# Kernel tuning notes

Hardware: AMD Instinct MI355X
Metric: run time of the kernel (lower is better)

Reference implementation:

```python
import jax, jax.numpy as jnp
import numpy as np
from jax import lax

B = 16
T_MEL = 16
FEAT = 80
BITS = 9
N_CLASSES = 2 ** BITS  # 512
RNN = 512
SCALES = (5, 5, 11)
PAD = 2
TOTAL_SCALE = 275      # prod(SCALES)
INDENT = PAD * TOTAL_SCALE  # 550
T = (T_MEL - 2 * PAD) * TOTAL_SCALE  # 3300
D_IN = FEAT + N_CLASSES  # 592 = GRU input size


def setup_inputs() -> dict:
    key = jax.random.key(0)
    ks = jax.random.split(key, 10)
    s = 0.05
    inp = {
        "x": jax.random.randint(ks[0], (B, T), 0, N_CLASSES),
        "mels": jax.random.normal(ks[1], (B, FEAT, T_MEL), jnp.float32),
    }
    # upsample conv kernels: Conv2d(1,1,(1,2s+1)) with weight filled 1/(2s+1)
    for i, sc in enumerate(SCALES):
        k = 2 * sc + 1
        inp[f"up_k{i}"] = jnp.full((1, 1, 1, k), 1.0 / k, jnp.float32)
    # GRU (torch layout: [3H, in], gates ordered r,z,n)
    inp["w_ih"] = jax.random.normal(ks[2], (3 * RNN, D_IN), jnp.float32) * s
    inp["w_hh"] = jax.random.normal(ks[3], (3 * RNN, RNN), jnp.float32) * s
    inp["b_ih"] = jax.random.normal(ks[4], (3 * RNN,), jnp.float32) * s
    inp["b_hh"] = jax.random.normal(ks[5], (3 * RNN,), jnp.float32) * s
    # fc1: Linear(rnn_dims, n_classes); fc2: Linear(n_classes, n_classes)
    inp["fc1_w"] = jax.random.normal(ks[6], (N_CLASSES, RNN), jnp.float32) * s
    inp["fc1_b"] = jax.random.normal(ks[7], (N_CLASSES,), jnp.float32) * s
    inp["fc2_w"] = jax.random.normal(ks[8], (N_CLASSES, N_CLASSES), jnp.float32) * s
    inp["fc2_b"] = jax.random.normal(ks[9], (N_CLASSES,), jnp.float32) * s
    return inp


def _upsample_mels(mels, kernels):
    # m-path of UpsampleNetwork: Stretch2d(scale,1) + averaging Conv2d per scale
    m = mels[:, None]  # [B,1,FEAT,T_MEL]
    for sc, k in zip(SCALES, kernels):
        m = jnp.repeat(m, sc, axis=-1)  # Stretch2d along time
        m = lax.conv_general_dilated(
            m, k, window_strides=(1, 1), padding=[(0, 0), (sc, sc)],
            dimension_numbers=("NCHW", "OIHW", "NCHW"))
    m = m[:, 0, :, INDENT:-INDENT]  # [B, FEAT, T]
    return jnp.transpose(m, (0, 2, 1))  # [B, T, FEAT]


def _gru(xin, w_ih, w_hh, b_ih, b_hh):
    # precompute input projection for all timesteps: [B,T,3H]
    x_proj = jnp.einsum("btd,gd->btg", xin, w_ih) + b_ih

    def step(h, xp):  # xp: [B,3H]
        hp = h @ w_hh.T + b_hh
        xr, xz, xn = jnp.split(xp, 3, axis=-1)
        hr, hz, hn = jnp.split(hp, 3, axis=-1)
        r = jax.nn.sigmoid(xr + hr)
        z = jax.nn.sigmoid(xz + hz)
        n = jnp.tanh(xn + r * hn)
        h_new = (1.0 - z) * n + z * h
        return h_new, h_new

    h0 = jnp.zeros((xin.shape[0], RNN), xin.dtype)
    _, hs = lax.scan(step, h0, jnp.transpose(x_proj, (1, 0, 2)))  # [T,B,H]
    return jnp.transpose(hs, (1, 0, 2))  # [B,T,H]


def reference(x, mels, up_k0, up_k1, up_k2,
              w_ih, w_hh, b_ih, b_hh, fc1_w, fc1_b, fc2_w, fc2_b):
    # vectorized replacement for the per-element scatter loop: one-hot of x
    netinput = jax.nn.one_hot(x, N_CLASSES, dtype=jnp.float32)  # [B,T,C]
    mels_up = _upsample_mels(mels, (up_k0, up_k1, up_k2))       # [B,T,FEAT]
    xin = jnp.concatenate([netinput, mels_up], axis=2)          # [B,T,C+FEAT]
    h = _gru(xin, w_ih, w_hh, b_ih, b_hh)                       # [B,T,RNN]
    h = jax.nn.relu(jnp.einsum("bth,fh->btf", h, fc1_w) + fc1_b)
    out = jnp.einsum("btf,cf->btc", h, fc2_w) + fc2_b           # [B,T,C]
    return out
```

## Files before the change

### kernel.cpp

```cpp
#include <hip/hip_runtime.h>
#include <stdint.h>

typedef unsigned short ushort_t;
typedef unsigned long long u64;
typedef __attribute__((ext_vector_type(8))) short short8;
typedef __attribute__((ext_vector_type(4))) float f32x4;

#define T_SEQ 3300
#define SENT 0x7FC00001u
#define SENTPAIR 0x7FC000017FC00001ull

__device__ __forceinline__ ushort_t f2b(float f) {
  uint32_t u = __float_as_uint(f);
  u = (u + 0x7fffu + ((u >> 16) & 1u)) >> 16;
  return (ushort_t)u;
}
__device__ __forceinline__ float b2f(ushort_t b) {
  return __uint_as_float(((uint32_t)b) << 16);
}

__global__ void prep_kernel(const float* __restrict__ w_ih,
                            const float* __restrict__ fc1w,
                            const float* __restrict__ fc2w,
                            ushort_t* __restrict__ w_ihT,
                            ushort_t* __restrict__ fc1wb,
                            ushort_t* __restrict__ fc2wb,
                            uint32_t* __restrict__ h_ring) {
  int i = blockIdx.x * 256 + threadIdx.x;
  if (i < 512 * 1536) {
    int d = i / 1536, g = i - d * 1536;
    w_ihT[i] = f2b(w_ih[g * 592 + d]);
  }
  int j = i - 512 * 1536;
  if (j >= 0 && j < 262144) fc1wb[j] = f2b(fc1w[j]);
  int k = j - 262144;
  if (k >= 0 && k < 262144) fc2wb[k] = f2b(fc2w[k]);
  int c = k - 262144;
  if (c >= 0 && c < 131072) {
    __hip_atomic_store(&h_ring[c], SENT, __ATOMIC_RELAXED, __HIP_MEMORY_SCOPE_AGENT);
  }
}

__global__ void upsample_kernel(const float* __restrict__ mels,
                                const float* __restrict__ k0,
                                const float* __restrict__ k1,
                                const float* __restrict__ k2,
                                float* __restrict__ mels_up) {
  __shared__ float s0[16];
  __shared__ float s1[80];
  __shared__ float s2[400];
  int bf = blockIdx.x;
  int b = bf / 80, f = bf - b * 80;
  int tid = threadIdx.x;
  float c0 = k0[0], c1 = k1[0], c2 = k2[0];
  if (tid < 16) s0[tid] = mels[(b * 80 + f) * 16 + tid];
  __syncthreads();
  if (tid < 80) {
    float a = 0.f;
    #pragma unroll
    for (int d = -5; d <= 5; ++d) {
      int w = tid + d;
      if (w >= 0 && w < 80) a += s0[w / 5];
    }
    s1[tid] = a * c0;
  }
  __syncthreads();
  for (int w = tid; w < 400; w += 128) {
    float a = 0.f;
    #pragma unroll
    for (int d = -5; d <= 5; ++d) {
      int u = w + d;
      if (u >= 0 && u < 400) a += s1[u / 5];
    }
    s2[w] = a * c1;
  }
  __syncthreads();
  for (int t = tid; t < T_SEQ; t += 128) {
    int wb = 550 + t;
    float a = 0.f;
    #pragma unroll
    for (int d = -11; d <= 11; ++d) a += s2[(wb + d) / 11];
    mels_up[(b * 80 + f) * T_SEQ + t] = a * c2;
  }
}

__device__ __forceinline__ float red32(float x) {
  x += __uint_as_float((uint32_t)__builtin_amdgcn_update_dpp(0, (int)__float_as_uint(x), 0x111, 0xf, 0xf, true));
  x += __uint_as_float((uint32_t)__builtin_amdgcn_update_dpp(0, (int)__float_as_uint(x), 0x112, 0xf, 0xf, true));
  x += __uint_as_float((uint32_t)__builtin_amdgcn_update_dpp(0, (int)__float_as_uint(x), 0x114, 0xf, 0xf, true));
  x += __uint_as_float((uint32_t)__builtin_amdgcn_update_dpp(0, (int)__float_as_uint(x), 0x118, 0xf, 0xf, true));
  x += __shfl_xor(x, 16, 64);
  return x;
}

__global__ __launch_bounds__(512) void gru_kernel(
    const int* __restrict__ x,
    const float* __restrict__ mels_up,
    const float* __restrict__ w_ih,
    const float* __restrict__ w_hh,
    const float* __restrict__ b_ih,
    const float* __restrict__ b_hh,
    const ushort_t* __restrict__ w_ihT,
    uint32_t* __restrict__ h_ring,
    ushort_t* __restrict__ h_seq)
{
  int blk = blockIdx.x;
  int xcd = blk & 7, slot = blk >> 3;
  int b = (xcd << 1) | (slot >> 4);
  int j = slot & 15;
  int tid = threadIdx.x;
  int cc = tid & 31, rr = tid >> 5;

  __shared__ __align__(16) float v[640];
  __shared__ float embs[96];

  if (tid < 48) v[592 + tid] = 0.f;

  float w[6][20];
  float wmel[2][3];
  float bsum[4], bihn[2], bhhn[2];
  #pragma unroll
  for (int q = 0; q < 6; ++q) {
    int gate = q >> 1, kk = q & 1;
    int g = gate * 512 + j * 32 + rr * 2 + kk;
    #pragma unroll
    for (int cl = 0; cl < 20; ++cl) {
      int col = cc * 20 + cl;
      float wv = 0.f;
      if (col < 512) wv = w_hh[g * 512 + col];
      else if (col < 592 && gate < 2) wv = w_ih[g * 592 + col];
      w[q][cl] = wv;
    }
  }
  #pragma unroll
  for (int kk = 0; kk < 2; ++kk) {
    int g = 1024 + j * 32 + rr * 2 + kk;
    #pragma unroll
    for (int ii = 0; ii < 3; ++ii) {
      int fidx = cc * 3 + ii;
      wmel[kk][ii] = (fidx < 80) ? w_ih[g * 592 + 512 + fidx] : 0.f;
    }
    bihn[kk] = b_ih[g];
    bhhn[kk] = b_hh[g];
  }
  #pragma unroll
  for (int q = 0; q < 4; ++q) {
    int gate = q >> 1, kk = q & 1;
    int g = gate * 512 + j * 32 + rr * 2 + kk;
    bsum[q] = b_ih[g] + b_hh[g];
  }

  for (int t = 0; t < T_SEQ; ++t) {
    float melv = 0.f;
    if (tid < 80) melv = mels_up[(b * 80 + tid) * T_SEQ + t];
    float embv = 0.f;
    if (tid < 96) {
      int xv = x[b * T_SEQ + t];
      int gate = tid >> 5, kl = tid & 31;
      embv = b2f(w_ihT[xv * 1536 + gate * 512 + j * 32 + kl]);
    }
    u64 q0 = 0, q1 = 0;
    if (t > 0 && tid < 128) {
      int rslot = (t - 1) & 15;
      const u64* src = (const u64*)&h_ring[((rslot * 16 + b) * 512) + tid * 4];
      for (;;) {
        q0 = __hip_atomic_load(src,     __ATOMIC_RELAXED, __HIP_MEMORY_SCOPE_AGENT);
        q1 = __hip_atomic_load(src + 1, __ATOMIC_RELAXED, __HIP_MEMORY_SCOPE_AGENT);
        if (((uint32_t)q0) != SENT && ((uint32_t)(q0 >> 32)) != SENT &&
            ((uint32_t)q1) != SENT && ((uint32_t)(q1 >> 32)) != SENT) break;
      }
    }
    if (tid < 128) {
      ((u64*)v)[tid * 2]     = q0;
      ((u64*)v)[tid * 2 + 1] = q1;
    }
    if (tid < 80) v[512 + tid] = melv;
    if (tid < 96) embs[tid] = embv;
    __syncthreads();

    float hv20[20];
    #pragma unroll
    for (int s = 0; s < 5; ++s) {
      f32x4 t4 = *(const f32x4*)&v[cc * 20 + s * 4];
      hv20[s * 4 + 0] = t4[0]; hv20[s * 4 + 1] = t4[1];
      hv20[s * 4 + 2] = t4[2]; hv20[s * 4 + 3] = t4[3];
    }
    float a0 = 0.f, a1 = 0.f, a2 = 0.f, a3 = 0.f, a4 = 0.f, a5 = 0.f;
    #pragma unroll
    for (int cl = 0; cl < 20; ++cl) {
      float hvv = hv20[cl];
      a0 += hvv * w[0][cl]; a1 += hvv * w[1][cl];
      a2 += hvv * w[2][cl]; a3 += hvv * w[3][cl];
      a4 += hvv * w[4][cl]; a5 += hvv * w[5][cl];
    }
    float am0 = 0.f, am1 = 0.f;
    #pragma unroll
    for (int ii = 0; ii < 3; ++ii) {
      float mv = v[512 + cc * 3 + ii];
      am0 += mv * wmel[0][ii]; am1 += mv * wmel[1][ii];
    }
    float r0 = red32(a0), r1 = red32(a1), r2 = red32(a2);
    float r3 = red32(a3), r4 = red32(a4), r5 = red32(a5);
    float rm0 = red32(am0), rm1 = red32(am1);

    if (cc == 15) {
      float hn2[2];
      #pragma unroll
      for (int kk = 0; kk < 2; ++kk) {
        float sr  = kk ? r1 : r0;
        float sz  = kk ? r3 : r2;
        float sn  = kk ? r5 : r4;
        float smn = kk ? rm1 : rm0;
        int k = rr * 2 + kk;
        float ar = embs[k] + sr + bsum[0 + kk];
        float az = embs[32 + k] + sz + bsum[2 + kk];
        float rg = 1.f / (1.f + __expf(-ar));
        float zg = 1.f / (1.f + __expf(-az));
        float xn = embs[64 + k] + smn + bihn[kk];
        float hn = sn + bhhn[kk];
        float na = xn + rg * hn;
        float e2 = __expf(2.f * na);
        float ng = 1.f - 2.f / (e2 + 1.f);
        float hp = v[j * 32 + k];
        hn2[kk] = (1.f - zg) * ng + zg * hp;
      }
      int wslot = t & 15;
      u64 pk = ((u64)__float_as_uint(hn2[1]) << 32) | (u64)__float_as_uint(hn2[0]);
      u64* dst = (u64*)&h_ring[((wslot * 16 + b) * 512) + j * 32 + rr * 2];
      __hip_atomic_store(dst, pk, __ATOMIC_RELAXED, __HIP_MEMORY_SCOPE_AGENT);
      int aslot = (t + 8) & 15;
      u64* adst = (u64*)&h_ring[((aslot * 16 + b) * 512) + j * 32 + rr * 2];
      __hip_atomic_store(adst, SENTPAIR, __ATOMIC_RELAXED, __HIP_MEMORY_SCOPE_AGENT);
      uint32_t hb = (uint32_t)f2b(hn2[0]) | ((uint32_t)f2b(hn2[1]) << 16);
      *(uint32_t*)&h_seq[(size_t)(b * T_SEQ + t) * 512 + j * 32 + rr * 2] = hb;
    }
    __syncthreads();
  }
}

__global__ __launch_bounds__(512) void head_kernel(
    const ushort_t* __restrict__ h_seq,
    const ushort_t* __restrict__ fc1w,
    const ushort_t* __restrict__ fc2w,
    const float* __restrict__ fc1b,
    const float* __restrict__ fc2b,
    float* __restrict__ out) {
  __shared__ __align__(16) ushort_t h1[64 * 512];
  int blk = blockIdx.x;
  int tid = threadIdx.x;
  int w = tid >> 6, l = tid & 63;
  int lm = l & 15, lq = l >> 4;
  int mt = w & 3;
  int nb = (w >> 2) * 256;
  int m0 = blk * 64;

  f32x4 acc[16];
  #pragma unroll
  for (int i = 0; i < 16; ++i) acc[i] = (f32x4){0.f, 0.f, 0.f, 0.f};
  const ushort_t* arow = h_seq + (size_t)(m0 + mt * 16 + lm) * 512;
  for (int kt = 0; kt < 16; ++kt) {
    short8 a = *(const short8*)(arow + kt * 32 + lq * 8);
    #pragma unroll
    for (int nt = 0; nt < 16; ++nt) {
      short8 bb = *(const short8*)(fc1w + (size_t)(nb + nt * 16 + lm) * 512 + kt * 32 + lq * 8);
      acc[nt] = __builtin_amdgcn_mfma_f32_16x16x32_bf16(a, bb, acc[nt], 0, 0, 0);
    }
  }
  #pragma unroll
  for (int nt = 0; nt < 16; ++nt) {
    int n = nb + nt * 16 + lm;
    float bias = fc1b[n];
    #pragma unroll
    for (int r = 0; r < 4; ++r) {
      int m = mt * 16 + lq * 4 + r;
      float vv = acc[nt][r] + bias;
      vv = fmaxf(vv, 0.f);
      h1[m * 512 + n] = f2b(vv);
    }
  }
  __syncthreads();
  f32x4 acc2[16];
  #pragma unroll
  for (int i = 0; i < 16; ++i) acc2[i] = (f32x4){0.f, 0.f, 0.f, 0.f};
  for (int kt = 0; kt < 16; ++kt) {
    short8 a = *(const short8*)&h1[(mt * 16 + lm) * 512 + kt * 32 + lq * 8];
    #pragma unroll
    for (int nt = 0; nt < 16; ++nt) {
      short8 bb = *(const short8*)(fc2w + (size_t)(nb + nt * 16 + lm) * 512 + kt * 32 + lq * 8);
      acc2[nt] = __builtin_amdgcn_mfma_f32_16x16x32_bf16(a, bb, acc2[nt], 0, 0, 0);
    }
  }
  #pragma unroll
  for (int nt = 0; nt < 16; ++nt) {
    int n = nb + nt * 16 + lm;
    float bias = fc2b[n];
    #pragma unroll
    for (int r = 0; r < 4; ++r) {
      int m = mt * 16 + lq * 4 + r;
      out[(size_t)(m0 + m) * 512 + n] = acc2[nt][r] + bias;
    }
  }
}

extern "C" void kernel_launch(void* const* d_in, const int* in_sizes, int n_in,
                              void* d_out, int out_size, void* d_ws, size_t ws_size,
                              hipStream_t stream) {
  (void)in_sizes; (void)n_in; (void)out_size; (void)ws_size;
  const int*   x    = (const int*)d_in[0];
  const float* mels = (const float*)d_in[1];
  const float* k0   = (const float*)d_in[2];
  const float* k1   = (const float*)d_in[3];
  const float* k2   = (const float*)d_in[4];
  const float* w_ih = (const float*)d_in[5];
  const float* w_hh = (const float*)d_in[6];
  const float* b_ih = (const float*)d_in[7];
  const float* b_hh = (const float*)d_in[8];
  const float* fc1w = (const float*)d_in[9];
  const float* fc1b = (const float*)d_in[10];
  const float* fc2w = (const float*)d_in[11];
  const float* fc2b = (const float*)d_in[12];

  char* ws = (char*)d_ws;
  float*    mels_up = (float*)(ws + 0);
  ushort_t* h_seq   = (ushort_t*)(ws + 16896000);
  ushort_t* w_ihT   = (ushort_t*)(ws + 70963200);
  ushort_t* fc1wb   = (ushort_t*)(ws + 72536064);
  ushort_t* fc2wb   = (ushort_t*)(ws + 73060352);
  uint32_t* h_ring  = (uint32_t*)(ws + 73584640);

  prep_kernel<<<5632, 256, 0, stream>>>(w_ih, fc1w, fc2w, w_ihT, fc1wb, fc2wb, h_ring);
  upsample_kernel<<<1280, 128, 0, stream>>>(mels, k0, k1, k2, mels_up);
  gru_kernel<<<256, 512, 0, stream>>>(x, mels_up, w_ih, w_hh, b_ih, b_hh, w_ihT,
                                      h_ring, h_seq);
  head_kernel<<<825, 512, 0, stream>>>(h_seq, fc1wb, fc2wb, fc1b, fc2b, (float*)d_out);
}
```

Measured before the change: 6.766 ms.

## Probe XCD-local coherence and use L2-scoped ring traffic for GRU handoff

At start, the 16 blocks sharing a batch row run a timed runtime probe that checks whether stores made with sc0 (L2-coherent, not device-coherent) are visible to their peers. If all peers agree, the per-step hidden-state ring loads and stores use inline-asm sc0 global loads and stores instead of agent-scope atomics, avoiding device-scope coherence cost on the serial critical path. The GRU matvec is also rewritten with two-wide float vectors so the compiler can emit packed FMA. This adds a startup handshake and relies on the block-to-XCD mapping assumption; if the probe passes spuriously, results could go stale.

```diff
diff --git a/kernel.cpp b/kernel.cpp
--- a/kernel.cpp
+++ b/kernel.cpp
@@ -5,6 +5,7 @@
 typedef unsigned long long u64;
 typedef __attribute__((ext_vector_type(8))) short short8;
 typedef __attribute__((ext_vector_type(4))) float f32x4;
+typedef __attribute__((ext_vector_type(2))) float f32x2;
 
 #define T_SEQ 3300
 #define SENT 0x7FC00001u
@@ -17,6 +18,25 @@
 }
 __device__ __forceinline__ float b2f(ushort_t b) {
   return __uint_as_float(((uint32_t)b) << 16);
+}
+
+__device__ __forceinline__ f32x4 ld16_loc(const void* p) {
+  f32x4 r;
+  asm volatile("global_load_dwordx4 %0, %1, off sc0\n\ts_waitcnt vmcnt(0)"
+               : "=v"(r) : "v"(p) : "memory");
+  return r;
+}
+__device__ __forceinline__ uint32_t ld32_loc(const void* p) {
+  uint32_t r;
+  asm volatile("global_load_dword %0, %1, off sc0\n\ts_waitcnt vmcnt(0)"
+               : "=v"(r) : "v"(p) : "memory");
+  return r;
+}
+__device__ __forceinline__ void st32_loc(void* p, uint32_t v) {
+  asm volatile("global_store_dword %0, %1, off sc0" :: "v"(p), "v"(v) : "memory");
+}
+__device__ __forceinline__ void st8_loc(void* p, u64 v) {
+  asm volatile("global_store_dwordx2 %0, %1, off sc0" :: "v"(p), "v"(v) : "memory");
 }
 
 __global__ void prep_kernel(const float* __restrict__ w_ih,
@@ -25,7 +45,8 @@
                             ushort_t* __restrict__ w_ihT,
                             ushort_t* __restrict__ fc1wb,
                             ushort_t* __restrict__ fc2wb,
-                            uint32_t* __restrict__ h_ring) {
+                            uint32_t* __restrict__ h_ring,
+                            uint32_t* __restrict__ pctl) {
   int i = blockIdx.x * 256 + threadIdx.x;
   if (i < 512 * 1536) {
     int d = i / 1536, g = i - d * 1536;
@@ -38,6 +59,10 @@
   int c = k - 262144;
   if (c >= 0 && c < 131072) {
     __hip_atomic_store(&h_ring[c], SENT, __ATOMIC_RELAXED, __HIP_MEMORY_SCOPE_AGENT);
+  }
+  int c2 = c - 131072;
+  if (c2 >= 0 && c2 < 768) {
+    __hip_atomic_store(&pctl[c2], SENT, __ATOMIC_RELAXED, __HIP_MEMORY_SCOPE_AGENT);
   }
 }
 
@@ -102,6 +127,7 @@
     const float* __restrict__ b_hh,
     const ushort_t* __restrict__ w_ihT,
     uint32_t* __restrict__ h_ring,
+    uint32_t* __restrict__ pctl,
     ushort_t* __restrict__ h_seq)
 {
   int blk = blockIdx.x;
@@ -113,10 +139,11 @@
 
   __shared__ __align__(16) float v[640];
   __shared__ float embs[96];
+  __shared__ int s_local;
 
   if (tid < 48) v[592 + tid] = 0.f;
 
-  float w[6][20];
+  f32x2 w2[6][10];
   float wmel[2][3];
   float bsum[4], bihn[2], bhhn[2];
   #pragma unroll
@@ -124,12 +151,17 @@
     int gate = q >> 1, kk = q & 1;
     int g = gate * 512 + j * 32 + rr * 2 + kk;
     #pragma unroll
-    for (int cl = 0; cl < 20; ++cl) {
-      int col = cc * 20 + cl;
-      float wv = 0.f;
-      if (col < 512) wv = w_hh[g * 512 + col];
-      else if (col < 592 && gate < 2) wv = w_ih[g * 592 + col];
-      w[q][cl] = wv;
+    for (int cl = 0; cl < 10; ++cl) {
+      f32x2 wv = {0.f, 0.f};
+      #pragma unroll
+      for (int e = 0; e < 2; ++e) {
+        int col = cc * 20 + cl * 2 + e;
+        float val = 0.f;
+        if (col < 512) val = w_hh[g * 512 + col];
+        else if (col < 592 && gate < 2) val = w_ih[g * 592 + col];
+        wv[e] = val;
+      }
+      w2[q][cl] = wv;
     }
   }
   #pragma unroll
@@ -149,6 +181,36 @@
     int g = gate * 512 + j * 32 + rr * 2 + kk;
     bsum[q] = b_ih[g] + b_hh[g];
   }
+
+  if (tid == 0) {
+    uint32_t* sync0 = pctl + b * 16;
+    uint32_t* probe = pctl + 256 + b * 16;
+    uint32_t* verd  = pctl + 512 + b * 16;
+    __hip_atomic_store(&sync0[j], 1u, __ATOMIC_RELAXED, __HIP_MEMORY_SCOPE_AGENT);
+    for (int kq = 0; kq < 16; ++kq)
+      while (__hip_atomic_load(&sync0[kq], __ATOMIC_RELAXED, __HIP_MEMORY_SCOPE_AGENT) == SENT) {}
+    st32_loc(&probe[j], 1u);
+    u64 t0 = __builtin_amdgcn_s_memrealtime();
+    int ok = 0;
+    for (;;) {
+      int seen = 1;
+      for (int kq = 0; kq < 16; ++kq)
+        if (ld32_loc(&probe[kq]) == SENT) { seen = 0; break; }
+      if (seen) { ok = 1; break; }
+      if (__builtin_amdgcn_s_memrealtime() - t0 > 4000) break;
+    }
+    __hip_atomic_store(&verd[j], ok ? 1u : 2u, __ATOMIC_RELAXED, __HIP_MEMORY_SCOPE_AGENT);
+    int allok = 1;
+    for (int kq = 0; kq < 16; ++kq) {
+      uint32_t vv;
+      do { vv = __hip_atomic_load(&verd[kq], __ATOMIC_RELAXED, __HIP_MEMORY_SCOPE_AGENT); }
+      while (vv == SENT);
+      if (vv != 1u) allok = 0;
+    }
+    s_local = allok;
+  }
+  __syncthreads();
+  int local = s_local;
 
   for (int t = 0; t < T_SEQ; ++t) {
     float melv = 0.f;
@@ -159,40 +221,54 @@
       int gate = tid >> 5, kl = tid & 31;
       embv = b2f(w_ihT[xv * 1536 + gate * 512 + j * 32 + kl]);
     }
-    u64 q0 = 0, q1 = 0;
+    f32x4 hq = {0.f, 0.f, 0.f, 0.f};
     if (t > 0 && tid < 128) {
       int rslot = (t - 1) & 15;
-      const u64* src = (const u64*)&h_ring[((rslot * 16 + b) * 512) + tid * 4];
-      for (;;) {
-        q0 = __hip_atomic_load(src,     __ATOMIC_RELAXED, __HIP_MEMORY_SCOPE_AGENT);
-        q1 = __hip_atomic_load(src + 1, __ATOMIC_RELAXED, __HIP_MEMORY_SCOPE_AGENT);
-        if (((uint32_t)q0) != SENT && ((uint32_t)(q0 >> 32)) != SENT &&
-            ((uint32_t)q1) != SENT && ((uint32_t)(q1 >> 32)) != SENT) break;
+      const uint32_t* src = &h_ring[((rslot * 16 + b) * 512) + tid * 4];
+      if (local) {
+        for (;;) {
+          hq = ld16_loc(src);
+          if (__float_as_uint(hq[0]) != SENT && __float_as_uint(hq[1]) != SENT &&
+              __float_as_uint(hq[2]) != SENT && __float_as_uint(hq[3]) != SENT) break;
+        }
+      } else {
+        const u64* s8 = (const u64*)src;
+        u64 q0, q1;
+        for (;;) {
+          q0 = __hip_atomic_load(s8,     __ATOMIC_RELAXED, __HIP_MEMORY_SCOPE_AGENT);
+          q1 = __hip_atomic_load(s8 + 1, __ATOMIC_RELAXED, __HIP_MEMORY_SCOPE_AGENT);
+          if (((uint32_t)q0) != SENT && ((uint32_t)(q0 >> 32)) != SENT &&
+              ((uint32_t)q1) != SENT && ((uint32_t)(q1 >> 32)) != SENT) break;
+        }
+        hq[0] = __uint_as_float((uint32_t)q0);
+        hq[1] = __uint_as_float((uint32_t)(q0 >> 32));
+        hq[2] = __uint_as_float((uint32_t)q1);
+        hq[3] = __uint_as_float((uint32_t)(q1 >> 32));
       }
     }
-    if (tid < 128) {
-      ((u64*)v)[tid * 2]     = q0;
-      ((u64*)v)[tid * 2 + 1] = q1;
-    }
+    if (tid < 128) *(f32x4*)&v[tid * 4] = hq;
     if (tid < 80) v[512 + tid] = melv;
     if (tid < 96) embs[tid] = embv;
     __syncthreads();
 
-    float hv20[20];
+    f32x2 hv2[10];
     #pragma unroll
     for (int s = 0; s < 5; ++s) {
       f32x4 t4 = *(const f32x4*)&v[cc * 20 + s * 4];
-      hv20[s * 4 + 0] = t4[0]; hv20[s * 4 + 1] = t4[1];
-      hv20[s * 4 + 2] = t4[2]; hv20[s * 4 + 3] = t4[3];
-    }
-    float a0 = 0.f, a1 = 0.f, a2 = 0.f, a3 = 0.f, a4 = 0.f, a5 = 0.f;
-    #pragma unroll
-    for (int cl = 0; cl < 20; ++cl) {
-      float hvv = hv20[cl];
-      a0 += hvv * w[0][cl]; a1 += hvv * w[1][cl];
-      a2 += hvv * w[2][cl]; a3 += hvv * w[3][cl];
-      a4 += hvv * w[4][cl]; a5 += hvv * w[5][cl];
-    }
+      hv2[s * 2]     = (f32x2){t4[0], t4[1]};
+      hv2[s * 2 + 1] = (f32x2){t4[2], t4[3]};
+    }
+    f32x2 p0 = {0.f,0.f}, p1 = {0.f,0.f}, p2 = {0.f,0.f};
+    f32x2 p3 = {0.f,0.f}, p4 = {0.f,0.f}, p5 = {0.f,0.f};
+    #pragma unroll
+    for (int cl = 0; cl < 10; ++cl) {
+      f32x2 hvv = hv2[cl];
+      p0 += hvv * w2[0][cl]; p1 += hvv * w2[1][cl];
+      p2 += hvv * w2[2][cl]; p3 += hvv * w2[3][cl];
+      p4 += hvv * w2[4][cl]; p5 += hvv * w2[5][cl];
+    }
+    float a0 = p0[0] + p0[1], a1 = p1[0] + p1[1], a2 = p2[0] + p2[1];
+    float a3 = p3[0] + p3[1], a4 = p4[0] + p4[1], a5 = p5[0] + p5[1];
     float am0 = 0.f, am1 = 0.f;
     #pragma unroll
     for (int ii = 0; ii < 3; ++ii) {
@@ -225,12 +301,17 @@
         hn2[kk] = (1.f - zg) * ng + zg * hp;
       }
       int wslot = t & 15;
+      int aslot = (t + 8) & 15;
       u64 pk = ((u64)__float_as_uint(hn2[1]) << 32) | (u64)__float_as_uint(hn2[0]);
-      u64* dst = (u64*)&h_ring[((wslot * 16 + b) * 512) + j * 32 + rr * 2];
-      __hip_atomic_store(dst, pk, __ATOMIC_RELAXED, __HIP_MEMORY_SCOPE_AGENT);
-      int aslot = (t + 8) & 15;
+      u64* dst  = (u64*)&h_ring[((wslot * 16 + b) * 512) + j * 32 + rr * 2];
       u64* adst = (u64*)&h_ring[((aslot * 16 + b) * 512) + j * 32 + rr * 2];
-      __hip_atomic_store(adst, SENTPAIR, __ATOMIC_RELAXED, __HIP_MEMORY_SCOPE_AGENT);
+      if (local) {
+        st8_loc(dst, pk);
+        st8_loc(adst, SENTPAIR);
+      } else {
+        __hip_atomic_store(dst,  pk,       __ATOMIC_RELAXED, __HIP_MEMORY_SCOPE_AGENT);
+        __hip_atomic_store(adst, SENTPAIR, __ATOMIC_RELAXED, __HIP_MEMORY_SCOPE_AGENT);
+      }
       uint32_t hb = (uint32_t)f2b(hn2[0]) | ((uint32_t)f2b(hn2[1]) << 16);
       *(uint32_t*)&h_seq[(size_t)(b * T_SEQ + t) * 512 + j * 32 + rr * 2] = hb;
     }
@@ -327,10 +408,12 @@
   ushort_t* fc1wb   = (ushort_t*)(ws + 72536064);
   ushort_t* fc2wb   = (ushort_t*)(ws + 73060352);
   uint32_t* h_ring  = (uint32_t*)(ws + 73584640);
-
-  prep_kernel<<<5632, 256, 0, stream>>>(w_ih, fc1w, fc2w, w_ihT, fc1wb, fc2wb, h_ring);
+  uint32_t* pctl    = (uint32_t*)(ws + 74108928);
+
+  prep_kernel<<<5635, 256, 0, stream>>>(w_ih, fc1w, fc2w, w_ihT, fc1wb, fc2wb,
+                                        h_ring, pctl);
   upsample_kernel<<<1280, 128, 0, stream>>>(mels, k0, k1, k2, mels_up);
   gru_kernel<<<256, 512, 0, stream>>>(x, mels_up, w_ih, w_hh, b_ih, b_hh, w_ihT,
-                                      h_ring, h_seq);
+                                      h_ring, pctl, h_seq);
   head_kernel<<<825, 512, 0, stream>>>(h_seq, fc1wb, fc2wb, fc1b, fc2b, (float*)d_out);
 }
```

After: 7.204 ms. +6.5%, slower.
